# Optimization experiments

Measured on AMD Instinct MI355X. Metric: run time of the kernel, lower is better.

## Reference

```python
import jax, jax.numpy as jnp
import numpy as np

HEADS = 16


def setup_inputs() -> dict:
    key = jax.random.key(0)
    k1, k2, k3, k4, k5, k6 = jax.random.split(key, 6)
    L, B, H = 1024, 8, 2048
    dk = H // HEADS
    std = 1.0 / np.sqrt(H)
    return {
        "query": jax.random.normal(k1, (B, H), dtype=jnp.float32),
        "feed_hiddens": jax.random.normal(k2, (L, B, H), dtype=jnp.float32),
        "values": jax.random.normal(k3, (L, B, H), dtype=jnp.float32),
        # additive-attention params (reconstructed from forward's shape constraints)
        "attn_w": jax.random.normal(k4, (2 * dk, H), dtype=jnp.float32) * std,
        "bias": jax.random.normal(k5, (H,), dtype=jnp.float32) * std,
        "score": jax.random.normal(k6, (H, 1), dtype=jnp.float32) * std,
    }


def reference(query, feed_hiddens, values, attn_w, bias, score):
    L, B, H = feed_hiddens.shape
    dk = H // HEADS
    # q: [B, h, 1, dk]; k, v: [B, h, L, dk]
    q = query.reshape(B, HEADS, 1, dk)
    k = feed_hiddens.reshape(L, B, HEADS, dk).transpose(1, 2, 0, 3)
    v = values.reshape(L, B, HEADS, dk).transpose(1, 2, 0, 3)
    # cat([q_rep, k], -1) @ attn_w  ==  q @ Wq + k @ Wk  (avoids the repeat/concat blowup)
    Wq, Wk = attn_w[:dk], attn_w[dk:]
    energy = jax.nn.relu(q @ Wq + k @ Wk + bias)        # [B, h, L, H]
    logits = (energy @ score).transpose(0, 1, 3, 2)     # [B, h, 1, L]
    a = jax.nn.softmax(logits, axis=-1)
    out = (a @ v).reshape(B, H)[None]                   # [1, B, H]
    return out
```

## Files before the change

### kernel.cpp

```cpp
#include <hip/hip_runtime.h>
#include <hip/hip_bf16.h>
#include <hip/hip_fp8.h>

#define HEADS 16
#define B_    8
#define H_    2048
#define L_    1024
#define DK    128

typedef __attribute__((ext_vector_type(8))) int   i32x8;
typedef __attribute__((ext_vector_type(4))) int   i32x4;
typedef __attribute__((ext_vector_type(4))) float f32x4;

__device__ __forceinline__ unsigned u8e4m3(float x) {
  __hip_fp8_e4m3 f8(x);
  return (unsigned)f8.__x;
}

__device__ __forceinline__ void gload_lds16(const void* g, void* l) {
  __builtin_amdgcn_global_load_lds(
      (const __attribute__((address_space(1))) void*)g,
      (__attribute__((address_space(3))) void*)l, 16, 0, 0);
}

__global__ void __launch_bounds__(256)
prep_kernel(const float* __restrict__ query,
            const float* __restrict__ attn_w,
            const float* __restrict__ bias,
            const float* __restrict__ score,
            unsigned* __restrict__ qsp,
            unsigned char* __restrict__ wk8) {
  const int tid = threadIdx.x;
  if (blockIdx.x < 128) {
    const int jt = blockIdx.x & 7;
    const int bg = blockIdx.x >> 3;
    __shared__ float qv[8][DK];
    for (int i = tid; i < 8 * DK; i += 256) {
      const int bh = bg * 8 + (i >> 7);
      const int d  = i & 127;
      const int b = bh >> 4, head = bh & 15;
      qv[i >> 7][d] = query[b * H_ + head * DK + d];
    }
    __syncthreads();
    const int j = jt * 256 + tid;
    const float bj = bias[j];
    const unsigned short us =
        __builtin_bit_cast(unsigned short, (__bf16)(score[j] * (1.0f / 64.0f)));
    float acc[8];
#pragma unroll
    for (int u = 0; u < 8; ++u) acc[u] = bj;
    for (int d = 0; d < DK; ++d) {
      const float wv = attn_w[d * H_ + j];
#pragma unroll
      for (int u = 0; u < 8; ++u) acc[u] += qv[u][d] * wv;
    }
#pragma unroll
    for (int u = 0; u < 8; ++u) {
      const unsigned short uq =
          __builtin_bit_cast(unsigned short, (__bf16)(64.0f * acc[u]));
      qsp[(size_t)(bg * 8 + u) * H_ + j] = ((unsigned)uq << 16) | us;
    }
  } else {
    const int t0 = (blockIdx.x - 128) * 256 + tid;
    for (int tt = t0; tt < 8192; tt += 4096) {
      const int l  = tt & 63;
      const int nc = tt >> 6;
      const int n  = nc * 16 + (l & 15);
      const int k0 = (l >> 4) * 32;
#pragma unroll
      for (int half = 0; half < 2; ++half) {
        unsigned w[4];
#pragma unroll
        for (int j = 0; j < 4; ++j) {
          unsigned v = 0;
#pragma unroll
          for (int byt = 0; byt < 4; ++byt) {
            const int i = half * 16 + j * 4 + byt;
            const float x = 64.0f * attn_w[(size_t)(DK + k0 + i) * H_ + n];
            v |= u8e4m3(x) << (8 * byt);
          }
          w[j] = v;
        }
        uint4 q; q.x = w[0]; q.y = w[1]; q.z = w[2]; q.w = w[3];
        *(uint4*)(wk8 + (size_t)nc * 2048 + half * 1024 + l * 16) = q;
      }
    }
  }
}

__global__ void __launch_bounds__(256, 2)
logits_kernel(const float* __restrict__ feed,
              const unsigned char* __restrict__ wk8,
              const unsigned* __restrict__ qsp,
              float* __restrict__ logits) {
  const int ltile = blockIdx.x;
  const int bh    = blockIdx.y;
  const int nblk  = blockIdx.z;
  const int b     = bh >> 4;
  const int head  = bh & 15;
  const int tid   = threadIdx.x;
  const int wave  = tid >> 6;
  const int lane  = tid & 63;
  const int row   = lane & 15;
  const int g     = lane >> 4;

  __shared__ unsigned char ring[4][8192];
  __shared__ unsigned qsl[1024];

#pragma unroll
  for (int u = 0; u < 4; ++u)
    qsl[tid + 256 * u] = qsp[(size_t)bh * H_ + nblk * 1024 + tid + 256 * u];

  i32x8 aF[4];
#pragma unroll
  for (int s = 0; s < 4; ++s) {
    const int l = ltile * 256 + wave * 64 + s * 16 + row;
    const float* fh = feed + (size_t)l * (B_ * H_) + b * H_ + head * DK + g * 32;
    i32x8 af;
#pragma unroll
    for (int j = 0; j < 8; ++j) {
      float4 x = *(const float4*)(fh + j * 4);
      unsigned v = u8e4m3(x.x) | (u8e4m3(x.y) << 8) |
                   (u8e4m3(x.z) << 16) | (u8e4m3(x.w) << 24);
      af[j] = (int)v;
    }
    aF[s] = af;
  }
  __syncthreads();

  const char* wkb   = (const char*)wk8 + (size_t)nblk * 131072;
  char*       ringb = (char*)ring;

#pragma unroll
  for (int ph = 0; ph < 2; ++ph) {
#pragma unroll
    for (int i = 0; i < 2; ++i)
      gload_lds16(wkb + (size_t)ph * 8192 + wave * 2048 + i * 1024 + lane * 16,
                  ringb + ph * 8192 + wave * 2048 + i * 1024);
  }

  float lacc[4][4] = {};

#pragma unroll 1
  for (int p = 0; p < 16; ++p) {
    const int pf = (p + 2 < 16) ? p + 2 : 15;
    const int ws = ((p + 2) & 3) * 8192;
    gload_lds16(wkb + (size_t)pf * 8192 + wave * 2048 + 0    + lane * 16,
                ringb + ws + wave * 2048 + 0);
    gload_lds16(wkb + (size_t)pf * 8192 + wave * 2048 + 1024 + lane * 16,
                ringb + ws + wave * 2048 + 1024);

    __builtin_amdgcn_sched_barrier(0);
    asm volatile("s_waitcnt vmcnt(4)" ::: "memory");
    __builtin_amdgcn_s_barrier();
    __builtin_amdgcn_sched_barrier(0);

    const char* rs = ringb + (p & 3) * 8192;
#pragma unroll
    for (int cc = 0; cc < 4; ++cc) {
      const char* rc = rs + cc * 2048 + lane * 16;
      i32x4 lo = *(const i32x4*)(rc);
      i32x4 hi = *(const i32x4*)(rc + 1024);
      i32x8 b8;
      b8[0] = lo[0]; b8[1] = lo[1]; b8[2] = lo[2]; b8[3] = lo[3];
      b8[4] = hi[0]; b8[5] = hi[1]; b8[6] = hi[2]; b8[7] = hi[3];
      const unsigned qu = qsl[(4 * p + cc) * 16 + row];
      const float qx = __uint_as_float(qu & 0xffff0000u);
      const float qy = __uint_as_float(qu << 16);

      f32x4 d0 = {qx, qx, qx, qx};
      f32x4 d1 = {qx, qx, qx, qx};
      f32x4 d2 = {qx, qx, qx, qx};
      f32x4 d3 = {qx, qx, qx, qx};
      d0 = __builtin_amdgcn_mfma_scale_f32_16x16x128_f8f6f4(
             aF[0], b8, d0, 0, 0, 0, 0x7F7F7F7F, 0, 0x7F7F7F7F);
      d1 = __builtin_amdgcn_mfma_scale_f32_16x16x128_f8f6f4(
             aF[1], b8, d1, 0, 0, 0, 0x7F7F7F7F, 0, 0x7F7F7F7F);
      d2 = __builtin_amdgcn_mfma_scale_f32_16x16x128_f8f6f4(
             aF[2], b8, d2, 0, 0, 0, 0x7F7F7F7F, 0, 0x7F7F7F7F);
      d3 = __builtin_amdgcn_mfma_scale_f32_16x16x128_f8f6f4(
             aF[3], b8, d3, 0, 0, 0, 0x7F7F7F7F, 0, 0x7F7F7F7F);

#pragma unroll
      for (int i = 0; i < 4; ++i) {
        lacc[0][i] += fmaxf(d0[i], 0.f) * qy;
        lacc[1][i] += fmaxf(d1[i], 0.f) * qy;
        lacc[2][i] += fmaxf(d2[i], 0.f) * qy;
        lacc[3][i] += fmaxf(d3[i], 0.f) * qy;
      }
    }
  }

#pragma unroll
  for (int s = 0; s < 4; ++s) {
#pragma unroll
    for (int i = 0; i < 4; ++i) {
      float v = lacc[s][i];
#pragma unroll
      for (int off = 1; off < 16; off <<= 1) v += __shfl_xor(v, off);
      lacc[s][i] = v;
    }
  }
  if (row == 0) {
    float* lout = logits + (size_t)nblk * (128 * L_);
#pragma unroll
    for (int s = 0; s < 4; ++s) {
      const int base = bh * L_ + ltile * 256 + wave * 64 + s * 16 + g * 4;
#pragma unroll
      for (int i = 0; i < 4; ++i) lout[base + i] = lacc[s][i];
    }
  }
}

__global__ void __launch_bounds__(256)
softmax_pv_kernel(const float* __restrict__ logits,
                  const float* __restrict__ values,
                  float* __restrict__ out) {
  const int bh    = blockIdx.x;
  const int dpart = blockIdx.y;
  const int b     = bh >> 4;
  const int head  = bh & 15;
  const int tid   = threadIdx.x;

  __shared__ float  sl[L_];
  __shared__ float  sred[4];
  __shared__ float  sscal;
  __shared__ float4 pacc[32][8];

  float m = -1e30f;
  for (int i = tid; i < L_; i += 256) {
    float v = logits[(size_t)bh * L_ + i] +
              logits[(size_t)(128 * L_) + bh * L_ + i];
    sl[i] = v;
    m = fmaxf(m, v);
  }
#pragma unroll
  for (int off = 32; off > 0; off >>= 1) m = fmaxf(m, __shfl_xor(m, off));
  if ((tid & 63) == 0) sred[tid >> 6] = m;
  __syncthreads();
  if (tid == 0) {
    float mm = fmaxf(fmaxf(sred[0], sred[1]), fmaxf(sred[2], sred[3]));
    sscal = mm;
  }
  __syncthreads();
  const float mx = sscal;

  float s = 0.f;
  for (int i = tid; i < L_; i += 256) {
    float e = __expf(sl[i] - mx);
    sl[i] = e;
    s += e;
  }
#pragma unroll
  for (int off = 32; off > 0; off >>= 1) s += __shfl_xor(s, off);
  if ((tid & 63) == 0) sred[tid >> 6] = s;
  __syncthreads();
  if (tid == 0) {
    sscal = 1.0f / ((sred[0] + sred[1]) + (sred[2] + sred[3]));
  }
  __syncthreads();
  const float inv = sscal;

  const int dq4  = tid & 7;
  const int lsub = tid >> 3;
  const float4* vp = (const float4*)(values + (size_t)b * H_ + head * DK + dpart * 32) + dq4;
  float4 acc = {0.f, 0.f, 0.f, 0.f};
  for (int ll = lsub; ll < L_; ll += 32) {
    const float w = sl[ll];
    float4 v = vp[(size_t)ll * (B_ * H_ / 4)];
    acc.x += w * v.x; acc.y += w * v.y; acc.z += w * v.z; acc.w += w * v.w;
  }
  pacc[lsub][dq4] = acc;
  __syncthreads();
  if (tid < 64) {
    const int q = tid & 7, k = tid >> 3;
    float4 a0 = pacc[k][q], a1 = pacc[k + 8][q], a2 = pacc[k + 16][q], a3 = pacc[k + 24][q];
    float4 r;
    r.x = (a0.x + a1.x) + (a2.x + a3.x);
    r.y = (a0.y + a1.y) + (a2.y + a3.y);
    r.z = (a0.z + a1.z) + (a2.z + a3.z);
    r.w = (a0.w + a1.w) + (a2.w + a3.w);
    pacc[k][q] = r;
  }
  __syncthreads();
  if (tid < 8) {
    float4 t = {0.f, 0.f, 0.f, 0.f};
#pragma unroll
    for (int k = 0; k < 8; ++k) {
      float4 a = pacc[k][tid];
      t.x += a.x; t.y += a.y; t.z += a.z; t.w += a.w;
    }
    t.x *= inv; t.y *= inv; t.z *= inv; t.w *= inv;
    *(float4*)(out + (size_t)b * H_ + head * DK + dpart * 32 + tid * 4) = t;
  }
}

extern "C" void kernel_launch(void* const* d_in, const int* in_sizes, int n_in,
                              void* d_out, int out_size, void* d_ws, size_t ws_size,
                              hipStream_t stream) {
  const float* query  = (const float*)d_in[0];
  const float* feed   = (const float*)d_in[1];
  const float* values = (const float*)d_in[2];
  const float* attn_w = (const float*)d_in[3];
  const float* bias   = (const float*)d_in[4];
  const float* score  = (const float*)d_in[5];
  float* out = (float*)d_out;

  unsigned*      qsp    = (unsigned*)d_ws;
  unsigned char* wk8    = (unsigned char*)d_ws + (size_t)(B_ * HEADS * H_) * sizeof(unsigned);
  float*         logits = (float*)(wk8 + (size_t)H_ * DK);

  prep_kernel<<<144, 256, 0, stream>>>(query, attn_w, bias, score, qsp, wk8);
  logits_kernel<<<dim3(L_ / 256, B_ * HEADS, 2), 256, 0, stream>>>(feed, wk8, qsp, logits);
  softmax_pv_kernel<<<dim3(B_ * HEADS, 4), 256, 0, stream>>>(logits, values, out);
}
```

Baseline: 85.63 us.

## Give each wave a private LDS ring and drop block-wide barriers in logits loop

Before, the four waves loaded Wk chunks cooperatively into a shared LDS ring and hit a block-wide s_barrier every iteration. Now each wave streams every Wk chunk into its own 4-slot ring with a prefetch depth of 3 and waits only on its own vmcnt, so no barrier is needed. The point is to let waves drift apart and stop stalling on each other. In exchange, each wave now issues four times as many global-to-LDS loads, since every wave fetches the whole Wk block itself, which adds L2/global traffic.

```diff
diff --git a/kernel.cpp b/kernel.cpp
--- a/kernel.cpp
+++ b/kernel.cpp
@@ -104,7 +104,7 @@
   const int row   = lane & 15;
   const int g     = lane >> 4;
 
-  __shared__ unsigned char ring[4][8192];
+  __shared__ unsigned char ring[4][4][2048];
   __shared__ unsigned qsl[1024];
 
 #pragma unroll
@@ -127,67 +127,57 @@
     aF[s] = af;
   }
   __syncthreads();
-
-  const char* wkb   = (const char*)wk8 + (size_t)nblk * 131072;
-  char*       ringb = (char*)ring;
-
-#pragma unroll
-  for (int ph = 0; ph < 2; ++ph) {
-#pragma unroll
-    for (int i = 0; i < 2; ++i)
-      gload_lds16(wkb + (size_t)ph * 8192 + wave * 2048 + i * 1024 + lane * 16,
-                  ringb + ph * 8192 + wave * 2048 + i * 1024);
+  asm volatile("s_waitcnt vmcnt(0)" ::: "memory");
+
+  const char* wkb    = (const char*)wk8 + (size_t)nblk * 131072;
+  char*       myring = (char*)ring[wave];
+
+#pragma unroll
+  for (int c = 0; c < 3; ++c) {
+    gload_lds16(wkb + (size_t)c * 2048 + lane * 16,        myring + c * 2048);
+    gload_lds16(wkb + (size_t)c * 2048 + 1024 + lane * 16, myring + c * 2048 + 1024);
   }
 
   float lacc[4][4] = {};
 
-#pragma unroll 1
-  for (int p = 0; p < 16; ++p) {
-    const int pf = (p + 2 < 16) ? p + 2 : 15;
-    const int ws = ((p + 2) & 3) * 8192;
-    gload_lds16(wkb + (size_t)pf * 8192 + wave * 2048 + 0    + lane * 16,
-                ringb + ws + wave * 2048 + 0);
-    gload_lds16(wkb + (size_t)pf * 8192 + wave * 2048 + 1024 + lane * 16,
-                ringb + ws + wave * 2048 + 1024);
+#pragma unroll 4
+  for (int p = 0; p < 64; ++p) {
+    const int pf = (p + 3 < 64) ? p + 3 : 63;
+    char* wdst = myring + ((p + 3) & 3) * 2048;
+    gload_lds16(wkb + (size_t)pf * 2048 + lane * 16,        wdst);
+    gload_lds16(wkb + (size_t)pf * 2048 + 1024 + lane * 16, wdst + 1024);
 
     __builtin_amdgcn_sched_barrier(0);
-    asm volatile("s_waitcnt vmcnt(4)" ::: "memory");
-    __builtin_amdgcn_s_barrier();
+    asm volatile("s_waitcnt vmcnt(6)" ::: "memory");
     __builtin_amdgcn_sched_barrier(0);
 
-    const char* rs = ringb + (p & 3) * 8192;
-#pragma unroll
-    for (int cc = 0; cc < 4; ++cc) {
-      const char* rc = rs + cc * 2048 + lane * 16;
-      i32x4 lo = *(const i32x4*)(rc);
-      i32x4 hi = *(const i32x4*)(rc + 1024);
-      i32x8 b8;
-      b8[0] = lo[0]; b8[1] = lo[1]; b8[2] = lo[2]; b8[3] = lo[3];
-      b8[4] = hi[0]; b8[5] = hi[1]; b8[6] = hi[2]; b8[7] = hi[3];
-      const unsigned qu = qsl[(4 * p + cc) * 16 + row];
-      const float qx = __uint_as_float(qu & 0xffff0000u);
-      const float qy = __uint_as_float(qu << 16);
-
-      f32x4 d0 = {qx, qx, qx, qx};
-      f32x4 d1 = {qx, qx, qx, qx};
-      f32x4 d2 = {qx, qx, qx, qx};
-      f32x4 d3 = {qx, qx, qx, qx};
-      d0 = __builtin_amdgcn_mfma_scale_f32_16x16x128_f8f6f4(
-             aF[0], b8, d0, 0, 0, 0, 0x7F7F7F7F, 0, 0x7F7F7F7F);
-      d1 = __builtin_amdgcn_mfma_scale_f32_16x16x128_f8f6f4(
-             aF[1], b8, d1, 0, 0, 0, 0x7F7F7F7F, 0, 0x7F7F7F7F);
-      d2 = __builtin_amdgcn_mfma_scale_f32_16x16x128_f8f6f4(
-             aF[2], b8, d2, 0, 0, 0, 0x7F7F7F7F, 0, 0x7F7F7F7F);
-      d3 = __builtin_amdgcn_mfma_scale_f32_16x16x128_f8f6f4(
-             aF[3], b8, d3, 0, 0, 0, 0x7F7F7F7F, 0, 0x7F7F7F7F);
-
-#pragma unroll
-      for (int i = 0; i < 4; ++i) {
-        lacc[0][i] += fmaxf(d0[i], 0.f) * qy;
-        lacc[1][i] += fmaxf(d1[i], 0.f) * qy;
-        lacc[2][i] += fmaxf(d2[i], 0.f) * qy;
-        lacc[3][i] += fmaxf(d3[i], 0.f) * qy;
-      }
+    const char* rc = myring + (p & 3) * 2048 + lane * 16;
+    i32x4 lo = *(const i32x4*)(rc);
+    i32x4 hi = *(const i32x4*)(rc + 1024);
+    i32x8 b8;
+    b8[0] = lo[0]; b8[1] = lo[1]; b8[2] = lo[2]; b8[3] = lo[3];
+    b8[4] = hi[0]; b8[5] = hi[1]; b8[6] = hi[2]; b8[7] = hi[3];
+    const unsigned qu = qsl[p * 16 + row];
+    const float qx = __uint_as_float(qu & 0xffff0000u);
+    const float qy = __uint_as_float(qu << 16);
+
+    const f32x4 dini = {qx, qx, qx, qx};
+    f32x4 d0, d1, d2, d3;
+    d0 = __builtin_amdgcn_mfma_scale_f32_16x16x128_f8f6f4(
+           aF[0], b8, dini, 0, 0, 0, 0x7F7F7F7F, 0, 0x7F7F7F7F);
+    d1 = __builtin_amdgcn_mfma_scale_f32_16x16x128_f8f6f4(
+           aF[1], b8, dini, 0, 0, 0, 0x7F7F7F7F, 0, 0x7F7F7F7F);
+    d2 = __builtin_amdgcn_mfma_scale_f32_16x16x128_f8f6f4(
+           aF[2], b8, dini, 0, 0, 0, 0x7F7F7F7F, 0, 0x7F7F7F7F);
+    d3 = __builtin_amdgcn_mfma_scale_f32_16x16x128_f8f6f4(
+           aF[3], b8, dini, 0, 0, 0, 0x7F7F7F7F, 0, 0x7F7F7F7F);
+
+#pragma unroll
+    for (int i = 0; i < 4; ++i) {
+      lacc[0][i] += fmaxf(d0[i], 0.f) * qy;
+      lacc[1][i] += fmaxf(d1[i], 0.f) * qy;
+      lacc[2][i] += fmaxf(d2[i], 0.f) * qy;
+      lacc[3][i] += fmaxf(d3[i], 0.f) * qy;
     }
   }
 
```

After: 90.47 us. 1.06x slower.
